# Performance work log

Hardware: AMD Instinct MI355X
Metric: run time of the kernel (lower is better)

## Reference

```python
import math
import jax, jax.numpy as jnp
import numpy as np

D_MODEL = 1024
N_HEADS = 16
HEAD_DIM = D_MODEL // N_HEADS
ROPE_THETA = 10000.0


def setup_inputs() -> dict:
    key = jax.random.key(0)
    ks = jax.random.split(key, 5)
    B, T = 4, 2048
    # xavier-ish scale for weights
    w_scale = math.sqrt(2.0 / (D_MODEL + D_MODEL))
    return {
        "x": jax.random.normal(ks[0], (B, T, D_MODEL), dtype=jnp.float32),
        "Wq": jax.random.normal(ks[1], (D_MODEL, D_MODEL), dtype=jnp.float32) * w_scale,
        "Wk": jax.random.normal(ks[2], (D_MODEL, D_MODEL), dtype=jnp.float32) * w_scale,
        "Wv": jax.random.normal(ks[3], (D_MODEL, D_MODEL), dtype=jnp.float32) * w_scale,
        "Wo": jax.random.normal(ks[4], (D_MODEL, D_MODEL), dtype=jnp.float32) * w_scale,
    }


def _apply_rope(t, offset=0):
    # t: (B, H, T, Dh); standard half-rotation RoPE
    B, H, T, Dh = t.shape
    inv_freq = 1.0 / (ROPE_THETA ** (jnp.arange(0, Dh, 2, dtype=jnp.float32) / Dh))
    pos = jnp.arange(T, dtype=jnp.float32) + offset  # (T,)
    ang = pos[:, None] * inv_freq[None, :]           # (T, Dh/2)
    cos = jnp.concatenate([jnp.cos(ang), jnp.cos(ang)], axis=-1)  # (T, Dh)
    sin = jnp.concatenate([jnp.sin(ang), jnp.sin(ang)], axis=-1)
    t1, t2 = t[..., : Dh // 2], t[..., Dh // 2 :]
    rot = jnp.concatenate([-t2, t1], axis=-1)
    return t * cos + rot * sin


def _forward(x, Wq, Wk, Wv, Wo):
    B, T, _ = x.shape
    scale = 1.0 / math.sqrt(HEAD_DIM)

    def split_heads(y):  # (B,T,D) -> (B,H,T,Dh)
        return y.reshape(B, T, N_HEADS, HEAD_DIM).transpose(0, 2, 1, 3)

    q = split_heads(x @ Wq.T)
    k = split_heads(x @ Wk.T)
    v = split_heads(x @ Wv.T)

    q = _apply_rope(q)
    k = _apply_rope(k)

    # full materialized scores, as in the original manual SDPA
    scores = jnp.einsum("bhtd,bhsd->bhts", q, k) * scale  # (B,H,T,T)
    causal = jnp.triu(jnp.ones((T, T), dtype=bool), k=1)   # True = masked
    scores = jnp.where(causal[None, None], -jnp.inf, scores)
    attn = jax.nn.softmax(scores, axis=-1)
    attn = jnp.nan_to_num(attn, nan=0.0)
    out = jnp.einsum("bhts,bhsd->bhtd", attn, v)           # (B,H,T,Dh)
    out = out.transpose(0, 2, 1, 3).reshape(B, T, N_HEADS * HEAD_DIM)
    return out @ Wo.T


def reference(x, Wq, Wk, Wv, Wo):
    return _forward(x, Wq, Wk, Wv, Wo)
```

## Files before the change

kernel.cpp:

```cpp
#include <hip/hip_runtime.h>
#include <math.h>

typedef __bf16 bf16_t;
typedef __bf16 bf16x4 __attribute__((ext_vector_type(4)));
typedef __bf16 bf16x8 __attribute__((ext_vector_type(8)));
typedef float f32x4 __attribute__((ext_vector_type(4)));

#define MFMA16(a, b, c) __builtin_amdgcn_mfma_f32_16x16x32_bf16(a, b, c, 0, 0, 0)
#define GLD_LDS16(g, l)                                                                    \
    __builtin_amdgcn_global_load_lds((const __attribute__((address_space(1))) void*)(g),   \
                                     (__attribute__((address_space(3))) void*)(l), 16, 0, 0)

#define SM_SCALE_LOG2E 0.18033688011112042f
#define NEG_LOG2_10K_32 -0.41524101186092029f

#define SWZ(r, u) ((((r) << 6) + (u)) ^ ((((r) >> 1) & 7) << 4))

__device__ __forceinline__ void fast_sincos(float ang, float* s, float* c) {
    float rev = ang * 0.15915494309189535f;
    rev = rev - floorf(rev);
    *s = __builtin_amdgcn_sinf(rev);
    *c = __builtin_amdgcn_cosf(rev);
}

__global__ void cvt_all(const float* __restrict__ x, const float* __restrict__ wq,
                        const float* __restrict__ wk, const float* __restrict__ wv,
                        const float* __restrict__ wo, bf16_t* __restrict__ out) {
    long i = ((long)blockIdx.x * 256 + threadIdx.x) * 4;
    const float* src;
    long off;
    const long M1 = 1048576;
    if (i < 8 * M1) { src = x;  off = i; }
    else if (i < 9 * M1)  { src = wq; off = i - 8 * M1; }
    else if (i < 10 * M1) { src = wk; off = i - 9 * M1; }
    else if (i < 11 * M1) { src = wv; off = i - 10 * M1; }
    else                  { src = wo; off = i - 11 * M1; }
    float4 v = *(const float4*)(src + off);
    out[i + 0] = (bf16_t)v.x;
    out[i + 1] = (bf16_t)v.y;
    out[i + 2] = (bf16_t)v.z;
    out[i + 3] = (bf16_t)v.w;
}

template <typename OutT>
__global__ __launch_bounds__(256) void gemm_bt(const bf16_t* __restrict__ A,
                                               const bf16_t* __restrict__ B,
                                               OutT* __restrict__ C,
                                               int M, int N, int K) {
    __shared__ __align__(16) bf16_t As[128 * 32];
    __shared__ __align__(16) bf16_t Bs[128 * 32];
    const int tid = threadIdx.x;
    const int lane = tid & 63, wave = tid >> 6;
    const int qd = lane >> 4, ln = lane & 15;
    const int m0 = blockIdx.y * 128, n0 = blockIdx.x * 128;
    const int wr = (wave >> 1) * 64, wc = (wave & 1) * 64;
    const int Kb = K * 2;

    f32x4 acc[4][4];
#pragma unroll
    for (int i = 0; i < 4; ++i)
#pragma unroll
        for (int j = 0; j < 4; ++j)
#pragma unroll
            for (int r = 0; r < 4; ++r) acc[i][j][r] = 0.f;

    const int off0 = wave * 2048 + lane * 16;
    const int off1 = off0 + 1024;
    const int r0 = off0 >> 6, c0 = off0 & 63;
    const int r1 = off1 >> 6, c1 = off1 & 63;

    for (int kt = 0; kt < K; kt += 32) {
        const char* Ab = (const char*)A + (size_t)m0 * Kb + kt * 2;
        const char* Bb = (const char*)B + (size_t)n0 * Kb + kt * 2;
        GLD_LDS16(Ab + (size_t)r0 * Kb + c0, (char*)As + wave * 2048);
        GLD_LDS16(Ab + (size_t)r1 * Kb + c1, (char*)As + wave * 2048 + 1024);
        GLD_LDS16(Bb + (size_t)r0 * Kb + c0, (char*)Bs + wave * 2048);
        GLD_LDS16(Bb + (size_t)r1 * Kb + c1, (char*)Bs + wave * 2048 + 1024);
        __syncthreads();
        bf16x8 af[4], bfr[4];
#pragma unroll
        for (int i = 0; i < 4; ++i)
            af[i] = *(const bf16x8*)(As + (wr + i * 16 + ln) * 32 + qd * 8);
#pragma unroll
        for (int j = 0; j < 4; ++j)
            bfr[j] = *(const bf16x8*)(Bs + (wc + j * 16 + ln) * 32 + qd * 8);
#pragma unroll
        for (int i = 0; i < 4; ++i)
#pragma unroll
            for (int j = 0; j < 4; ++j)
                acc[i][j] = MFMA16(af[i], bfr[j], acc[i][j]);
        __syncthreads();
    }
#pragma unroll
    for (int i = 0; i < 4; ++i)
#pragma unroll
        for (int j = 0; j < 4; ++j)
#pragma unroll
            for (int r = 0; r < 4; ++r) {
                int row = m0 + wr + i * 16 + qd * 4 + r;
                int col = n0 + wc + j * 16 + ln;
                C[(size_t)row * N + col] = (OutT)acc[i][j][r];
            }
}

__global__ __launch_bounds__(512) void gemm_qkv_rope8(const bf16_t* __restrict__ A,
                                                      const bf16_t* __restrict__ B,
                                                      bf16_t* __restrict__ Qo,
                                                      bf16_t* __restrict__ Ko,
                                                      bf16_t* __restrict__ Vt) {
    __shared__ __align__(16) bf16_t LA[2][2][256 * 32];
    __shared__ __align__(16) bf16_t LB[2][2][256 * 32];
    const int tid = threadIdx.x;
    const int wave = tid >> 6, lane = tid & 63;
    const int qd = lane >> 4, ln = lane & 15;
    const int wrr = wave >> 2, wcc = wave & 3;
    const int m0 = blockIdx.y * 256, n0 = blockIdx.x * 256;

    f32x4 acc[8][4];
#pragma unroll
    for (int m = 0; m < 8; ++m)
#pragma unroll
        for (int n = 0; n < 4; ++n)
#pragma unroll
            for (int r = 0; r < 4; ++r) acc[m][n][r] = 0.f;

    const int soff = wave * 1024 + lane * 16;
    const int slog = soff ^ (((soff >> 7) & 7) << 4);
    const int srow = slog >> 6;
    const int scol = slog & 63;
    const char* Abase = (const char*)A + (size_t)(m0 + srow) * 2048 + scol;
    const char* Bbase = (const char*)B + (size_t)(n0 + srow) * 2048 + scol;

    int aoff[8], boff[4];
#pragma unroll
    for (int m = 0; m < 8; ++m) {
        int r = m * 32 + wrr * 16 + ln;
        aoff[m] = ((r << 6) + (qd << 4)) ^ (((r >> 1) & 7) << 4);
    }
#pragma unroll
    for (int n = 0; n < 4; ++n) {
        int r = wcc * 64 + n * 16 + ln;
        boff[n] = ((r << 6) + (qd << 4)) ^ (((r >> 1) & 7) << 4);
    }

    auto stageA = [&](int kt, int kh, int nb) {
        const char* g = Abase + kt * 128 + kh * 64;
        char* l = (char*)&LA[nb][kh][0] + wave * 1024;
        GLD_LDS16(g, l);
        GLD_LDS16(g + (size_t)128 * 2048, l + 8192);
    };
    auto stageB = [&](int kt, int kh, int nb) {
        const char* g = Bbase + kt * 128 + kh * 64;
        char* l = (char*)&LB[nb][kh][0] + wave * 1024;
        GLD_LDS16(g, l);
        GLD_LDS16(g + (size_t)128 * 2048, l + 8192);
    };

    bf16x8 fA[4], fB[4];
#define LOAD_B(kh, bb_)                                          \
    {                                                            \
        const char* base_ = (const char*)&LB[bb_][kh][0];        \
        fB[0] = *(const bf16x8*)(base_ + boff[0]);               \
        fB[1] = *(const bf16x8*)(base_ + boff[1]);               \
        fB[2] = *(const bf16x8*)(base_ + boff[2]);               \
        fB[3] = *(const bf16x8*)(base_ + boff[3]);               \
    }
#define LOAD_A(mh, kh, bb_)                                      \
    {                                                            \
        const char* base_ = (const char*)&LA[bb_][kh][0];        \
        fA[0] = *(const bf16x8*)(base_ + aoff[(mh)*4 + 0]);      \
        fA[1] = *(const bf16x8*)(base_ + aoff[(mh)*4 + 1]);      \
        fA[2] = *(const bf16x8*)(base_ + aoff[(mh)*4 + 2]);      \
        fA[3] = *(const bf16x8*)(base_ + aoff[(mh)*4 + 3]);      \
    }
#define MFMA_Q(mh)                                                               \
    {                                                                            \
        __builtin_amdgcn_s_setprio(1);                                           \
        _Pragma("unroll") for (int mm = 0; mm < 4; ++mm)                         \
            _Pragma("unroll") for (int nn = 0; nn < 4; ++nn)                     \
                acc[(mh)*4 + mm][nn] = MFMA16(fA[mm], fB[nn], acc[(mh)*4 + mm][nn]); \
        __builtin_amdgcn_s_setprio(0);                                           \
    }
#define BAR __builtin_amdgcn_s_barrier()
#define WAIT_LGKM asm volatile("s_waitcnt lgkmcnt(0)" ::: "memory")

    stageB(0, 0, 0);
    stageA(0, 0, 0);
    stageB(0, 1, 0);
    stageA(0, 1, 0);
    asm volatile("s_waitcnt vmcnt(4)" ::: "memory");
    BAR;

    int buf = 0;
    for (int kt = 0; kt < 16; ++kt) {
        const int nb = buf ^ 1;
        const bool pre = (kt + 1 < 16);
        LOAD_B(0, buf);
        LOAD_A(0, 0, buf);
        if (pre) stageB(kt + 1, 0, nb);
        BAR;
        WAIT_LGKM;
        MFMA_Q(0);
        BAR;
        LOAD_A(1, 0, buf);
        if (pre) stageA(kt + 1, 0, nb);
        BAR;
        WAIT_LGKM;
        MFMA_Q(1);
        if (pre) { asm volatile("s_waitcnt vmcnt(4)" ::: "memory"); }
        else     { asm volatile("s_waitcnt vmcnt(0)" ::: "memory"); }
        BAR;
        LOAD_B(1, buf);
        LOAD_A(0, 1, buf);
        if (pre) stageB(kt + 1, 1, nb);
        BAR;
        WAIT_LGKM;
        MFMA_Q(0);
        BAR;
        LOAD_A(1, 1, buf);
        if (pre) stageA(kt + 1, 1, nb);
        BAR;
        WAIT_LGKM;
        MFMA_Q(1);
        if (pre) { asm volatile("s_waitcnt vmcnt(4)" ::: "memory"); }
        else     { asm volatile("s_waitcnt vmcnt(0)" ::: "memory"); }
        BAR;
        buf = nb;
    }
#undef LOAD_B
#undef LOAD_A
#undef MFMA_Q
#undef BAR
#undef WAIT_LGKM

    if (n0 < 2048) {
        const bool isQ = (n0 < 1024);
        bf16_t* Out = isQ ? Qo : Ko;
        const float scale = isQ ? SM_SCALE_LOG2E : 1.0f;
        const int nc0 = (n0 & 1023) + wcc * 64;
        const float inv0 = exp2f((float)ln * NEG_LOG2_10K_32);
        const float inv1 = exp2f((float)(ln + 16) * NEG_LOG2_10K_32);
#pragma unroll
        for (int m = 0; m < 8; ++m) {
#pragma unroll
            for (int r = 0; r < 4; ++r) {
                int row = m0 + m * 32 + wrr * 16 + qd * 4 + r;
                int t = row & 2047, bb = row >> 11;
                float ft = (float)t;
                float s0, c0v, s1, c1v;
                fast_sincos(ft * inv0, &s0, &c0v);
                fast_sincos(ft * inv1, &s1, &c1v);
#pragma unroll
                for (int n = 0; n < 4; ++n) {
                    int col = nc0 + n * 16 + ln;
                    int h = col >> 6, d = col & 63;
                    float sv = (n & 1) ? s1 : s0;
                    float cv = (n & 1) ? c1v : c0v;
                    float td = acc[m][n][r], tp = acc[m][n ^ 2][r];
                    float o = (n < 2) ? (td * cv - tp * sv) : (td * cv + tp * sv);
                    Out[((size_t)(bb * 16 + h) * 2048 + t) * 64 + d] = (bf16_t)(o * scale);
                }
            }
        }
    } else {
        const int nv0 = (n0 - 2048) + wcc * 64;
#pragma unroll
        for (int m = 0; m < 8; ++m) {
            int tb = m0 + m * 32 + wrr * 16 + qd * 4;
            int t = tb & 2047, bb = tb >> 11;
#pragma unroll
            for (int n = 0; n < 4; ++n) {
                int col = nv0 + n * 16 + ln;
                int h = col >> 6, d = col & 63;
                bf16x4 pk;
#pragma unroll
                for (int r = 0; r < 4; ++r) pk[r] = (bf16_t)acc[m][n][r];
                *(bf16x4*)(Vt + ((size_t)(bb * 16 + h) * 64 + d) * 2048 + t) = pk;
            }
        }
    }
}

__global__ __launch_bounds__(256) void attn_fwd(const bf16_t* __restrict__ Qg,
                                                const bf16_t* __restrict__ Kg,
                                                const bf16_t* __restrict__ Vtg,
                                                bf16_t* __restrict__ Og) {
    __shared__ __align__(16) bf16_t Kt[2 * 64 * 32];
    __shared__ __align__(16) bf16_t Vl[2 * 64 * 32];
    __shared__ __align__(16) bf16_t Pl[4][2 * 32 * 32];
    const int id = blockIdx.x;
    const int bh = ((id & 7) << 3) | ((id >> 3) & 7);
    const int pair = (id >> 6) & 7;
    const int b = bh >> 4, h = bh & 15;
    const int tid = threadIdx.x, wave = tid >> 6, lane = tid & 63;
    const int qd = lane >> 4, ln = lane & 15;
    const int kr0r = tid >> 3, kr1r = 32 + (tid >> 3);
    const int ch = tid & 7;
    const int kr0c = ch * 8;
    const int wh = (ch >> 2) * 4096;
    const int wu = (ch & 3) << 4;
    const int wo0 = wh + SWZ(kr0r, wu);
    const int wo1 = wh + SWZ(kr1r, wu);
    const bf16_t* Kbh = Kg + (size_t)bh * 2048 * 64;
    const bf16_t* Vbh = Vtg + (size_t)bh * 64 * 2048;

    bf16x8 vones;
#pragma unroll
    for (int i = 0; i < 8; ++i) vones[i] = (bf16_t)1.0f;

    for (int ph = 0; ph < 2; ++ph) {
        const int qt = ph ? 15 - pair : pair;
        const int q0 = qt * 128;
        const int wrow = q0 + wave * 32;
        const int njt = 2 * qt + 2;

        bf16x8 aq[2][2];
#pragma unroll
        for (int f = 0; f < 2; ++f) {
            const bf16_t* Qbase = Qg + ((size_t)bh * 2048 + wrow + f * 16 + ln) * 64;
            aq[f][0] = *(const bf16x8*)(Qbase + qd * 8);
            aq[f][1] = *(const bf16x8*)(Qbase + 32 + qd * 8);
        }

        f32x4 lsum[2];
        f32x4 o_acc[2][4];
#pragma unroll
        for (int f = 0; f < 2; ++f) {
#pragma unroll
            for (int r = 0; r < 4; ++r) lsum[f][r] = 0.f;
#pragma unroll
            for (int c = 0; c < 4; ++c)
#pragma unroll
                for (int r = 0; r < 4; ++r) o_acc[f][c][r] = 0.f;
        }

        int4 kr0, kr1, vr0, vr1;
        auto issue = [&](int j) {
            const bf16_t* kp = Kbh + (size_t)j * 64 * 64;
            const bf16_t* vp = Vbh + j * 64;
            kr0 = *(const int4*)(kp + kr0r * 64 + kr0c);
            kr1 = *(const int4*)(kp + kr1r * 64 + kr0c);
            vr0 = *(const int4*)(vp + (size_t)kr0r * 2048 + kr0c);
            vr1 = *(const int4*)(vp + (size_t)kr1r * 2048 + kr0c);
        };
        issue(0);

        for (int j = 0; j < njt; ++j) {
            __syncthreads();
            *(int4*)((char*)Kt + wo0) = kr0;
            *(int4*)((char*)Kt + wo1) = kr1;
            *(int4*)((char*)Vl + wo0) = vr0;
            *(int4*)((char*)Vl + wo1) = vr1;
            __syncthreads();
            if (j + 1 < njt) issue(j + 1);

            if (j * 64 > wrow + 31) continue;
            const int j64 = j * 64;

            f32x4 s[2][4];
            __builtin_amdgcn_s_setprio(1);
#pragma unroll
            for (int st = 0; st < 4; ++st) {
                const int rk = st * 16 + ln;
                bf16x8 bk0 = *(const bf16x8*)((const char*)Kt + SWZ(rk, qd * 16));
                bf16x8 bk1 = *(const bf16x8*)((const char*)Kt + 4096 + SWZ(rk, qd * 16));
#pragma unroll
                for (int f = 0; f < 2; ++f) {
                    f32x4 t = {0.f, 0.f, 0.f, 0.f};
                    t = MFMA16(aq[f][0], bk0, t);
                    t = MFMA16(aq[f][1], bk1, t);
                    s[f][st] = t;
                }
            }
            __builtin_amdgcn_s_setprio(0);

            if (j64 + 63 <= wrow) {
#pragma unroll
                for (int f = 0; f < 2; ++f)
#pragma unroll
                    for (int st = 0; st < 4; ++st)
#pragma unroll
                        for (int r = 0; r < 4; ++r)
                            s[f][st][r] = __builtin_amdgcn_exp2f(s[f][st][r]);
            } else {
#pragma unroll
                for (int f = 0; f < 2; ++f) {
                    int rowb = wrow + f * 16 + qd * 4;
#pragma unroll
                    for (int st = 0; st < 4; ++st) {
                        int col = j64 + st * 16 + ln;
#pragma unroll
                        for (int r = 0; r < 4; ++r) {
                            float v = (col > rowb + r) ? -INFINITY : s[f][st][r];
                            s[f][st][r] = __builtin_amdgcn_exp2f(v);
                        }
                    }
                }
            }

            char* Pw = (char*)&Pl[wave][0];
#pragma unroll
            for (int f = 0; f < 2; ++f)
#pragma unroll
                for (int st = 0; st < 4; ++st) {
                    const int ph2 = (st >> 1) * 2048;
                    const int pu = ((st & 1) * 16 + ln) * 2;
#pragma unroll
                    for (int r = 0; r < 4; ++r) {
                        const int prow = f * 16 + qd * 4 + r;
                        *(bf16_t*)(Pw + ph2 + SWZ(prow, pu)) = (bf16_t)s[f][st][r];
                    }
                }

            bf16x8 bv[4][2];
#pragma unroll
            for (int ct = 0; ct < 4; ++ct) {
                const int rv = ct * 16 + ln;
                bv[ct][0] = *(const bf16x8*)((const char*)Vl + SWZ(rv, qd * 16));
                bv[ct][1] = *(const bf16x8*)((const char*)Vl + 4096 + SWZ(rv, qd * 16));
            }
            __builtin_amdgcn_s_setprio(1);
#pragma unroll
            for (int f = 0; f < 2; ++f) {
                const int rp = f * 16 + ln;
                bf16x8 ap0 = *(const bf16x8*)(Pw + SWZ(rp, qd * 16));
                bf16x8 ap1 = *(const bf16x8*)(Pw + 2048 + SWZ(rp, qd * 16));
                lsum[f] = MFMA16(ap0, vones, lsum[f]);
                lsum[f] = MFMA16(ap1, vones, lsum[f]);
#pragma unroll
                for (int ct = 0; ct < 4; ++ct) {
                    o_acc[f][ct] = MFMA16(ap0, bv[ct][0], o_acc[f][ct]);
                    o_acc[f][ct] = MFMA16(ap1, bv[ct][1], o_acc[f][ct]);
                }
            }
            __builtin_amdgcn_s_setprio(0);
        }

#pragma unroll
        for (int f = 0; f < 2; ++f) {
            size_t obase = ((size_t)b * 2048 + wrow + f * 16 + qd * 4) * 1024 + h * 64;
            float rl[4];
#pragma unroll
            for (int r = 0; r < 4; ++r) rl[r] = __builtin_amdgcn_rcpf(lsum[f][r]);
#pragma unroll
            for (int ct = 0; ct < 4; ++ct)
#pragma unroll
                for (int r = 0; r < 4; ++r)
                    Og[obase + (size_t)r * 1024 + ct * 16 + ln] =
                        (bf16_t)(o_acc[f][ct][r] * rl[r]);
        }
    }
}

extern "C" void kernel_launch(void* const* d_in, const int* in_sizes, int n_in,
                              void* d_out, int out_size, void* d_ws, size_t ws_size,
                              hipStream_t stream) {
    (void)in_sizes; (void)n_in; (void)out_size; (void)ws_size;
    const float* x  = (const float*)d_in[0];
    const float* Wq = (const float*)d_in[1];
    const float* Wk = (const float*)d_in[2];
    const float* Wv = (const float*)d_in[3];
    const float* Wo = (const float*)d_in[4];
    char* ws = (char*)d_ws;
    const size_t MB = 1ull << 20;
    bf16_t* xb   = (bf16_t*)(ws + 0);
    bf16_t* wqb  = (bf16_t*)(ws + 16 * MB);
    bf16_t* wob  = (bf16_t*)(ws + 22 * MB);
    bf16_t* Qb   = (bf16_t*)(ws + 24 * MB);
    bf16_t* Kb   = (bf16_t*)(ws + 40 * MB);
    bf16_t* Vtb  = (bf16_t*)(ws + 56 * MB);
    bf16_t* AOb  = xb;

    cvt_all<<<dim3(12288), dim3(256), 0, stream>>>(x, Wq, Wk, Wv, Wo, (bf16_t*)ws);

    gemm_qkv_rope8<<<dim3(12, 32), dim3(512), 0, stream>>>(xb, wqb, Qb, Kb, Vtb);

    attn_fwd<<<dim3(512), dim3(256), 0, stream>>>(Qb, Kb, Vtb, AOb);

    gemm_bt<float><<<dim3(8, 64), dim3(256), 0, stream>>>(AOb, wob, (float*)d_out, 8192, 1024, 1024);
}
```

Measured before the change: 258.0 us.

## Load K/V fragments directly from global into registers, drop LDS staging and barriers

The attention kernel no longer stages K and V tiles through shared memory with two block barriers per tile. Each wave now loads its MFMA operand fragments for K and V straight from global memory into registers, prefetching the next tile after its use. Each wave also stops at its own causal limit instead of looping to the block's tile count. This removes the barriers and LDS traffic and lets waves run independently. In exchange, the four waves each reload the same K/V tiles, which raises global/L2 traffic and register pressure, and the global access pattern is less coalesced.

```diff
diff --git a/kernel.cpp b/kernel.cpp
--- a/kernel.cpp
+++ b/kernel.cpp
@@ -285,8 +285,6 @@
                                                 const bf16_t* __restrict__ Kg,
                                                 const bf16_t* __restrict__ Vtg,
                                                 bf16_t* __restrict__ Og) {
-    __shared__ __align__(16) bf16_t Kt[2 * 64 * 32];
-    __shared__ __align__(16) bf16_t Vl[2 * 64 * 32];
     __shared__ __align__(16) bf16_t Pl[4][2 * 32 * 32];
     const int id = blockIdx.x;
     const int bh = ((id & 7) << 3) | ((id >> 3) & 7);
@@ -294,15 +292,8 @@
     const int b = bh >> 4, h = bh & 15;
     const int tid = threadIdx.x, wave = tid >> 6, lane = tid & 63;
     const int qd = lane >> 4, ln = lane & 15;
-    const int kr0r = tid >> 3, kr1r = 32 + (tid >> 3);
-    const int ch = tid & 7;
-    const int kr0c = ch * 8;
-    const int wh = (ch >> 2) * 4096;
-    const int wu = (ch & 3) << 4;
-    const int wo0 = wh + SWZ(kr0r, wu);
-    const int wo1 = wh + SWZ(kr1r, wu);
-    const bf16_t* Kbh = Kg + (size_t)bh * 2048 * 64;
-    const bf16_t* Vbh = Vtg + (size_t)bh * 64 * 2048;
+    const char* Kbh = (const char*)(Kg + (size_t)bh * 2048 * 64);
+    const char* Vbh = (const char*)(Vtg + (size_t)bh * 64 * 2048);
 
     bf16x8 vones;
 #pragma unroll
@@ -313,6 +304,8 @@
         const int q0 = qt * 128;
         const int wrow = q0 + wave * 32;
         const int njt = 2 * qt + 2;
+        const int nw = ((wrow + 31) >> 6) + 1;
+        const int njtw = (njt < nw) ? njt : nw;
 
         bf16x8 aq[2][2];
 #pragma unroll
@@ -334,45 +327,44 @@
                 for (int r = 0; r < 4; ++r) o_acc[f][c][r] = 0.f;
         }
 
-        int4 kr0, kr1, vr0, vr1;
-        auto issue = [&](int j) {
-            const bf16_t* kp = Kbh + (size_t)j * 64 * 64;
-            const bf16_t* vp = Vbh + j * 64;
-            kr0 = *(const int4*)(kp + kr0r * 64 + kr0c);
-            kr1 = *(const int4*)(kp + kr1r * 64 + kr0c);
-            vr0 = *(const int4*)(vp + (size_t)kr0r * 2048 + kr0c);
-            vr1 = *(const int4*)(vp + (size_t)kr1r * 2048 + kr0c);
+        bf16x8 nk[8], nv[8];
+        auto issueK = [&](int j) {
+            const char* kp = Kbh + (size_t)j * 8192;
+#pragma unroll
+            for (int st = 0; st < 4; ++st) {
+                const char* rp = kp + (st * 16 + ln) * 128 + qd * 16;
+                nk[2 * st]     = *(const bf16x8*)(rp);
+                nk[2 * st + 1] = *(const bf16x8*)(rp + 64);
+            }
         };
-        issue(0);
-
-        for (int j = 0; j < njt; ++j) {
-            __syncthreads();
-            *(int4*)((char*)Kt + wo0) = kr0;
-            *(int4*)((char*)Kt + wo1) = kr1;
-            *(int4*)((char*)Vl + wo0) = vr0;
-            *(int4*)((char*)Vl + wo1) = vr1;
-            __syncthreads();
-            if (j + 1 < njt) issue(j + 1);
-
-            if (j * 64 > wrow + 31) continue;
+        auto issueV = [&](int j) {
+#pragma unroll
+            for (int ct = 0; ct < 4; ++ct) {
+                const char* rp = Vbh + (size_t)(ct * 16 + ln) * 4096 + j * 128 + qd * 16;
+                nv[2 * ct]     = *(const bf16x8*)(rp);
+                nv[2 * ct + 1] = *(const bf16x8*)(rp + 64);
+            }
+        };
+        issueK(0);
+        issueV(0);
+
+        for (int j = 0; j < njtw; ++j) {
             const int j64 = j * 64;
 
             f32x4 s[2][4];
             __builtin_amdgcn_s_setprio(1);
 #pragma unroll
             for (int st = 0; st < 4; ++st) {
-                const int rk = st * 16 + ln;
-                bf16x8 bk0 = *(const bf16x8*)((const char*)Kt + SWZ(rk, qd * 16));
-                bf16x8 bk1 = *(const bf16x8*)((const char*)Kt + 4096 + SWZ(rk, qd * 16));
 #pragma unroll
                 for (int f = 0; f < 2; ++f) {
                     f32x4 t = {0.f, 0.f, 0.f, 0.f};
-                    t = MFMA16(aq[f][0], bk0, t);
-                    t = MFMA16(aq[f][1], bk1, t);
+                    t = MFMA16(aq[f][0], nk[2 * st], t);
+                    t = MFMA16(aq[f][1], nk[2 * st + 1], t);
                     s[f][st] = t;
                 }
             }
             __builtin_amdgcn_s_setprio(0);
+            if (j + 1 < njtw) issueK(j + 1);
 
             if (j64 + 63 <= wrow) {
 #pragma unroll
@@ -412,13 +404,6 @@
                     }
                 }
 
-            bf16x8 bv[4][2];
-#pragma unroll
-            for (int ct = 0; ct < 4; ++ct) {
-                const int rv = ct * 16 + ln;
-                bv[ct][0] = *(const bf16x8*)((const char*)Vl + SWZ(rv, qd * 16));
-                bv[ct][1] = *(const bf16x8*)((const char*)Vl + 4096 + SWZ(rv, qd * 16));
-            }
             __builtin_amdgcn_s_setprio(1);
 #pragma unroll
             for (int f = 0; f < 2; ++f) {
@@ -429,11 +414,12 @@
                 lsum[f] = MFMA16(ap1, vones, lsum[f]);
 #pragma unroll
                 for (int ct = 0; ct < 4; ++ct) {
-                    o_acc[f][ct] = MFMA16(ap0, bv[ct][0], o_acc[f][ct]);
-                    o_acc[f][ct] = MFMA16(ap1, bv[ct][1], o_acc[f][ct]);
+                    o_acc[f][ct] = MFMA16(ap0, nv[2 * ct], o_acc[f][ct]);
+                    o_acc[f][ct] = MFMA16(ap1, nv[2 * ct + 1], o_acc[f][ct]);
                 }
             }
             __builtin_amdgcn_s_setprio(0);
+            if (j + 1 < njtw) issueV(j + 1);
         }
 
 #pragma unroll
```

After: 317.7 us. 23.2% more time.
